# Kernel tuning notes

Hardware: AMD Instinct MI355X
Metric: run time of the kernel (lower is better)

## Reference

```python
import jax, jax.numpy as jnp
import numpy as np

N_VERTICES = 50000
N_RADIAL = 5
N_ANGULAR = 8
FEATURE_DIM = 64
AMT_TEMPLATES = 64
TEMPLATE_RADIUS = 0.03
ROTATION_DELTA = 1


def create_template_matrix(n_radial, n_angular, radius):
    # Polar grid of template vertices in cartesian coordinates: (R, A, 2)
    radii = radius * (np.arange(1, n_radial + 1) / n_radial)
    angles = 2.0 * np.pi * np.arange(n_angular) / n_angular
    x = radii[:, None] * np.cos(angles)[None, :]
    y = radii[:, None] * np.sin(angles)[None, :]
    return np.stack([x, y], axis=-1).astype(np.float32)


def define_interpolation_coefficients(template_matrix):
    # Gaussian interpolation prior (concrete instance of the abstract method),
    # normalized over all template vertices. Shape: (R, A, R, A)
    R, A, _ = template_matrix.shape
    flat = template_matrix.reshape(R * A, 2)
    d2 = ((flat[:, None, :] - flat[None, :, :]) ** 2).sum(-1)  # (RA, RA)
    sigma = TEMPLATE_RADIUS / N_RADIAL
    w = np.exp(-d2 / (2.0 * sigma ** 2))
    w = w / w.sum(axis=1, keepdims=True)
    return w.reshape(R, A, R, A).astype(np.float32)


def setup_inputs() -> dict:
    key = jax.random.key(0)
    k1, k2, k3, k4, k5, k6, k7 = jax.random.split(key, 7)
    mesh_signal = jax.random.normal(k1, (N_VERTICES, FEATURE_DIM), dtype=jnp.float32)
    # barycentric coordinates: [..., 0] = vertex index (stored as float),
    # [..., 1] = barycentric weight summing to 1 over the 3 triangle corners
    idx = jax.random.randint(k2, (N_VERTICES, N_RADIAL, N_ANGULAR, 3), 0, N_VERTICES)
    w = jax.random.uniform(k3, (N_VERTICES, N_RADIAL, N_ANGULAR, 3), dtype=jnp.float32)
    w = w / jnp.sum(w, axis=-1, keepdims=True)
    bary_coordinates = jnp.stack([idx.astype(jnp.float32), w], axis=-1)
    neighbor_weights = jax.random.normal(
        k4, (AMT_TEMPLATES, N_RADIAL, N_ANGULAR, FEATURE_DIM), dtype=jnp.float32) * 0.05
    center_weights = jax.random.normal(
        k5, (AMT_TEMPLATES, 1, FEATURE_DIM), dtype=jnp.float32) * 0.05
    bias = jax.random.normal(k6, (AMT_TEMPLATES,), dtype=jnp.float32) * 0.05
    tmpl = create_template_matrix(N_RADIAL, N_ANGULAR, TEMPLATE_RADIUS)
    interp_coeff = jnp.asarray(
        define_interpolation_coefficients(tmpl).reshape(N_RADIAL, N_ANGULAR, N_RADIAL * N_ANGULAR))
    return {
        "mesh_signal": mesh_signal,
        "bary_coordinates": bary_coordinates,
        "neighbor_weights": neighbor_weights,
        "center_weights": center_weights,
        "bias": bias,
        "interp_coeff": interp_coeff,
    }


def reference(mesh_signal, bary_coordinates, neighbor_weights, center_weights, bias, interp_coeff):
    N, R, A, _, _ = bary_coordinates.shape
    C = mesh_signal.shape[-1]
    T = neighbor_weights.shape[0]

    # ---- patch operator: barycentric gather + interpolation ----
    idx = bary_coordinates[..., 0].astype(jnp.int32)          # (N, R, A, 3)
    bw = bary_coordinates[..., 1]                              # (N, R, A, 3)
    gathered = mesh_signal[idx]                                # (N, R, A, 3, C)
    interp = jnp.sum(bw[..., None] * gathered, axis=-2)        # (N, R, A, C)

    # ---- prior: matvec with interpolation coefficients ----
    # original: (N,1,1,C,RA) matvec (R,A,RA) -> (N,R,A,C)
    ms = interp.reshape(N, R * A, C)                           # (N, RA, C)
    interp = jnp.einsum('nmc,ram->nrac', ms, interp_coeff)     # (N, R, A, C)

    # ---- center fold: einsum('si,tji->sjt') ----
    conv_center = jnp.einsum('nc,tjc->njt', mesh_signal, center_weights)  # (N, 1, T)

    # ---- neighbor fold over rotations ----
    # roll(interp, shift=r, axis=angular) . W == interp . roll(W, shift=-r, axis=angular)
    rotations = np.arange(0, A, ROTATION_DELTA)
    w_rot = jnp.stack([jnp.roll(neighbor_weights, -int(r), axis=2) for r in rotations])  # (O, T, R, A, C)
    conv_neighbor = jnp.einsum('nrac,otrac->not', interp, w_rot) + bias                  # (N, O, T)

    return jax.nn.relu(conv_center + conv_neighbor)
```

## Files before the change

### kernel.cpp

```cpp
#include <hip/hip_runtime.h>
#include <hip/hip_bf16.h>

#define N_V   50000
#define KTOT  2624
#define NOUT  512
#define NKB   41
#define BM    128
#define BN    256
#define KT32  82

typedef short v8s __attribute__((ext_vector_type(8)));
typedef float v4f __attribute__((ext_vector_type(4)));
typedef unsigned int v4u __attribute__((ext_vector_type(4)));
typedef unsigned short u16;
typedef unsigned int u32;

__device__ __forceinline__ u16 f2bf(float f) {
    u32 u = __float_as_uint(f);
    return (u16)((u + 0x7FFFu + ((u >> 16) & 1u)) >> 16);
}

__device__ __forceinline__ void gl2lds(const u16* g, u16* l) {
    __builtin_amdgcn_global_load_lds(
        (const __attribute__((address_space(1))) u32*)(uintptr_t)g,
        (__attribute__((address_space(3))) u32*)(uintptr_t)l, 16, 0, 0);
}

__device__ __forceinline__ u32 ipair(u32 pa, u32 pb, u32 pc, float w0, float w1, float w2) {
    float a0 = __uint_as_float(pa << 16), a1 = __uint_as_float(pa & 0xffff0000u);
    float b0 = __uint_as_float(pb << 16), b1 = __uint_as_float(pb & 0xffff0000u);
    float c0 = __uint_as_float(pc << 16), c1 = __uint_as_float(pc & 0xffff0000u);
    float r0 = w0 * a0 + w1 * b0 + w2 * c0;
    float r1 = w0 * a1 + w1 * b1 + w2 * c1;
    return __builtin_amdgcn_perm(__float_as_uint(r1) + 0x8000u,
                                 __float_as_uint(r0) + 0x8000u, 0x07060302u);
}

__global__ void cast_ms(const float* __restrict__ ms, u16* __restrict__ msb,
                        u16* __restrict__ Xc) {
    int i = (blockIdx.x * 256 + threadIdx.x) * 4;
    float4 v = *reinterpret_cast<const float4*>(ms + i);
    ushort4 o;
    o.x = f2bf(v.x); o.y = f2bf(v.y); o.z = f2bf(v.z); o.w = f2bf(v.w);
    *reinterpret_cast<ushort4*>(msb + i) = o;
    if (Xc) {
        int n = i >> 6, c = i & 63;
        *reinterpret_cast<ushort4*>(Xc + (size_t)n * KTOT + 2560 + c) = o;
    }
}

__global__ void build_w2(const float* __restrict__ nw, const float* __restrict__ cw,
                         const float* __restrict__ coeff, u16* __restrict__ w2) {
    int l = blockIdx.x * 256 + threadIdx.x;
    if (l >= NOUT * KTOT) return;
    int j = l / KTOT, k = l - j * KTOT;
    int o = j >> 6, t = j & 63;
    u16 v;
    if (k >= 2560) {
        v = f2bf(cw[t * 64 + (k - 2560)]);
    } else {
        int m = k >> 6, c = k & 63;
        float s = 0.f;
        #pragma unroll
        for (int ra = 0; ra < 40; ++ra) {
            int r = ra >> 3, a = ra & 7;
            s += coeff[ra * 40 + m] * nw[((t * 5 + r) * 8 + ((a + o) & 7)) * 64 + c];
        }
        v = f2bf(s);
    }
    w2[l] = v;
}

__global__ void build_x(const float* __restrict__ bary, const u16* __restrict__ msb,
                        u16* __restrict__ X) {
    u32 t = blockIdx.x * 256 + threadIdx.x;
    u32 n = t / 160u;
    u32 rem = t - n * 160u;
    u32 m = rem >> 2, j = rem & 3;
    const float* bb = bary + (size_t)n * 240 + m * 6;
    float2 p0 = *(const float2*)(bb);
    float2 p1 = *(const float2*)(bb + 2);
    float2 p2 = *(const float2*)(bb + 4);
    u32 jb = j * 32u;
    u32 o0 = ((u32)(int)p0.x) * 128u + jb;
    u32 o1 = ((u32)(int)p1.x) * 128u + jb;
    u32 o2 = ((u32)(int)p2.x) * 128u + jb;
    const char* mb = (const char*)msb;
    v4u a0 = *(const v4u*)(mb + o0), b0 = *(const v4u*)(mb + o0 + 16);
    v4u a1 = *(const v4u*)(mb + o1), b1 = *(const v4u*)(mb + o1 + 16);
    v4u a2 = *(const v4u*)(mb + o2), b2 = *(const v4u*)(mb + o2 + 16);
    v4u c0, c1;
    #pragma unroll
    for (int e = 0; e < 4; ++e) {
        c0[e] = ipair(a0[e], a1[e], a2[e], p0.y, p1.y, p2.y);
        c1[e] = ipair(b0[e], b1[e], b2[e], p0.y, p1.y, p2.y);
    }
    char* xp = (char*)X + (size_t)n * (KTOT * 2) + m * 128 + jb;
    *(v4u*)xp = c0;
    *(v4u*)(xp + 16) = c1;
}

#define WBAR(N) asm volatile("s_waitcnt vmcnt(" #N ")\n\ts_barrier" ::: "memory")

__global__ __launch_bounds__(512, 2)
void gemm3(const u16* __restrict__ X, const u16* __restrict__ w2,
           const float* __restrict__ bias, float* __restrict__ out) {
    extern __shared__ char lds[];

    const int tid  = threadIdx.x;
    const int lane = tid & 63, wave = tid >> 6;
    const int l15  = lane & 15, q = lane >> 4;
    const int wm   = wave >> 2, wn = wave & 3;

    const int id = blockIdx.x;
    const int p  = (id & 7) + 8 * (id >> 4);
    const int by = (id >> 3) & 1;
    if (p >= 196) return;
    const int row0 = p * 256, col0 = by * 256;

    u32 aoff[2], boff[2];
    #pragma unroll
    for (int h = 0; h < 2; ++h) {
        int slot = (wave * 2 + h) * 64 + lane;
        int row  = slot >> 2, b = slot & 3;
        int g    = b ^ ((row >> 1) & 3);
        int grow = row0 + row; if (grow > N_V - 1) grow = N_V - 1;
        aoff[h] = (u32)grow * (u32)KTOT + (u32)(g * 8);
        boff[h] = (u32)(col0 + row) * (u32)KTOT + (u32)(g * 8);
    }

    const int sw = (l15 >> 1) & 3;
    const u32 a_rd0 = (u32)(wm * 128 + l15) * 64u + (u32)((q ^ sw) * 16);
    const u32 b_rd0 = (u32)(wn * 64  + l15) * 64u + (u32)((q ^ sw) * 16);

    v4f acc[8][4];
    #pragma unroll
    for (int mi = 0; mi < 8; ++mi)
        #pragma unroll
        for (int ni = 0; ni < 4; ++ni)
            acc[mi][ni] = (v4f){0.f, 0.f, 0.f, 0.f};

#define STG(T, BUF) do { \
    const u32 _ko = (u32)(T) * 32u; \
    _Pragma("unroll") \
    for (int _h = 0; _h < 2; ++_h) { \
        gl2lds(X  + aoff[_h] + _ko, (u16*)(lds + (BUF) * 16384 + (wave * 2 + _h) * 1024)); \
        gl2lds(w2 + boff[_h] + _ko, (u16*)(lds + 65536 + (BUF) * 16384 + (wave * 2 + _h) * 1024)); \
    } } while (0)

#define CMP(BUF) do { \
    const char* _ap = lds + (BUF) * 16384; \
    const char* _bp = lds + 65536 + (BUF) * 16384; \
    v8s _bf[4], _af[8]; \
    _Pragma("unroll") \
    for (int _ni = 0; _ni < 4; ++_ni) _bf[_ni] = *(const v8s*)(_bp + b_rd0 + _ni * 1024); \
    _Pragma("unroll") \
    for (int _mi = 0; _mi < 8; ++_mi) _af[_mi] = *(const v8s*)(_ap + a_rd0 + _mi * 1024); \
    __builtin_amdgcn_s_setprio(1); \
    _Pragma("unroll") \
    for (int _mi = 0; _mi < 8; ++_mi) \
        _Pragma("unroll") \
        for (int _ni = 0; _ni < 4; ++_ni) \
            acc[_mi][_ni] = __builtin_amdgcn_mfma_f32_16x16x32_bf16( \
                _af[_mi], _bf[_ni], acc[_mi][_ni], 0, 0, 0); \
    __builtin_amdgcn_s_setprio(0); \
} while (0)

    STG(0, 0); STG(1, 1); STG(2, 2);

    #pragma unroll 1
    for (int t = 0; t < KT32 - 3; ++t) {
        WBAR(8);
        STG(t + 3, (t + 3) & 3);
        CMP(t & 3);
    }
    WBAR(8); CMP(3);
    WBAR(4); CMP(0);
    WBAR(0); CMP(1);

#undef STG
#undef CMP

    float bv[4];
    #pragma unroll
    for (int ni = 0; ni < 4; ++ni) bv[ni] = bias[ni * 16 + l15];
    #pragma unroll
    for (int mi = 0; mi < 8; ++mi) {
        int rbase = row0 + wm * 128 + mi * 16 + q * 4;
        #pragma unroll
        for (int ni = 0; ni < 4; ++ni) {
            int cg = col0 + wn * 64 + ni * 16 + l15;
            #pragma unroll
            for (int rg = 0; rg < 4; ++rg) {
                int rr = rbase + rg;
                if (rr < N_V) {
                    float v = acc[mi][ni][rg] + bv[ni];
                    out[(size_t)rr * NOUT + cg] = v > 0.f ? v : 0.f;
                }
            }
        }
    }
}

__global__ __launch_bounds__(512, 4)
void gemm2(const u16* __restrict__ X, const u16* __restrict__ w2,
           const float* __restrict__ bias, float* __restrict__ out) {
    __shared__ u16 At[BM * 64];
    __shared__ u16 Bt[BN * 64];

    const int tid  = threadIdx.x;
    const int lane = tid & 63, wave = tid >> 6;
    const int l15  = lane & 15, q = lane >> 4;
    const int wm   = wave >> 2, wn = wave & 3;

    const int id = blockIdx.x;
    const int p  = (id & 7) + 8 * (id >> 4);
    const int by = (id >> 3) & 1;
    if (p >= 391) return;
    const int row0 = p * BM, col0 = by * BN;

    u32 aoff[2];
    #pragma unroll
    for (int h = 0; h < 2; ++h) {
        int slot = wave * 128 + h * 64 + lane;
        int arow = slot >> 3, ablk = (slot & 7) ^ (arow & 7);
        int grow = row0 + arow; if (grow > N_V - 1) grow = N_V - 1;
        aoff[h] = (u32)grow * (u32)KTOT + (u32)(ablk * 8);
    }
    u32 boff[4];
    #pragma unroll
    for (int i = 0; i < 4; ++i) {
        int slot = wave * 256 + i * 64 + lane;
        int brow = slot >> 3, bblk = (slot & 7) ^ (brow & 7);
        boff[i] = (u32)(col0 + brow) * (u32)KTOT + (u32)(bblk * 8);
    }

    const int eq = l15 & 7;
    const u32 a_rd0 = (u32)(wm * 64 + l15) * 128 + (u32)((q ^ eq) * 16);
    const u32 b_rd0 = (u32)(wn * 64 + l15) * 128 + (u32)((q ^ eq) * 16);

    v4f acc[4][4];
    #pragma unroll
    for (int mi = 0; mi < 4; ++mi)
        #pragma unroll
        for (int ni = 0; ni < 4; ++ni)
            acc[mi][ni] = (v4f){0.f, 0.f, 0.f, 0.f};

    #pragma unroll 1
    for (int kb = 0; kb < NKB; ++kb) {
        __syncthreads();
        #pragma unroll
        for (int h = 0; h < 2; ++h)
            gl2lds(X + aoff[h] + kb * 64, &At[wave * 1024 + h * 512]);
        #pragma unroll
        for (int i = 0; i < 4; ++i)
            gl2lds(w2 + boff[i] + kb * 64, &Bt[wave * 2048 + i * 512]);
        __syncthreads();

        const char* atp = (const char*)At;
        const char* btp = (const char*)Bt;
        #pragma unroll
        for (int s = 0; s < 2; ++s) {
            u32 ao = a_rd0 ^ (u32)(s * 64), bo = b_rd0 ^ (u32)(s * 64);
            v8s a_f[4], b_f[4];
            #pragma unroll
            for (int mi = 0; mi < 4; ++mi) a_f[mi] = *(const v8s*)(atp + ao + mi * 2048);
            #pragma unroll
            for (int ni = 0; ni < 4; ++ni) b_f[ni] = *(const v8s*)(btp + bo + ni * 2048);
            #pragma unroll
            for (int mi = 0; mi < 4; ++mi)
                #pragma unroll
                for (int ni = 0; ni < 4; ++ni)
                    acc[mi][ni] = __builtin_amdgcn_mfma_f32_16x16x32_bf16(
                        a_f[mi], b_f[ni], acc[mi][ni], 0, 0, 0);
        }
    }

    float bv[4];
    #pragma unroll
    for (int ni = 0; ni < 4; ++ni) bv[ni] = bias[ni * 16 + l15];
    #pragma unroll
    for (int mi = 0; mi < 4; ++mi) {
        int rbase = row0 + wm * 64 + mi * 16 + q * 4;
        #pragma unroll
        for (int ni = 0; ni < 4; ++ni) {
            int cg = col0 + wn * 64 + ni * 16 + l15;
            #pragma unroll
            for (int rg = 0; rg < 4; ++rg) {
                int rr = rbase + rg;
                if (rr < N_V) {
                    float v = acc[mi][ni][rg] + bv[ni];
                    out[(size_t)rr * NOUT + cg] = v > 0.f ? v : 0.f;
                }
            }
        }
    }
}

__global__ __launch_bounds__(512, 2)
void gemm_fused(const float* __restrict__ bary, const u16* __restrict__ msb,
                const u16* __restrict__ w2, const float* __restrict__ bias,
                float* __restrict__ out) {
    __shared__ u16 At[BM * 64];
    __shared__ u16 Bt[2 * BN * 64];

    const int tid  = threadIdx.x;
    const int lane = tid & 63, wave = tid >> 6;
    const int l15  = lane & 15, q = lane >> 4;
    const int wm   = wave >> 2, wn = wave & 3;

    const int id  = blockIdx.x;
    const int bx  = id % 391, by = id / 391;
    const int row0 = bx * BM, col0 = by * BN;

    const int ar  = tid >> 2;
    const u32 acb = (u32)(tid & 3) * 32;
    int an = row0 + ar; if (an > N_V - 1) an = N_V - 1;
    const u32* brow = (const u32*)bary + (size_t)an * 240;
    const u32 an_off = (u32)an * 128 + acb;

    const int e_a = ar & 7;
    const u32 at_w0 = (u32)ar * 128 + (u32)(((2 * (tid & 3)) ^ e_a) * 16);
    const u32 at_w1 = at_w0 ^ 16;

    const int eq = l15 & 7;
    const u32 a_rd0 = (u32)(wm * 64 + l15) * 128 + (u32)((q ^ eq) * 16);
    const u32 b_rd0 = (u32)(wn * 64 + l15) * 128 + (u32)((q ^ eq) * 16);

    const int rl = lane >> 3;
    const int bl = (lane & 7) ^ rl;

    v4f acc[4][4];
    #pragma unroll
    for (int mi = 0; mi < 4; ++mi)
        #pragma unroll
        for (int ni = 0; ni < 4; ++ni)
            acc[mi][ni] = (v4f){0.f, 0.f, 0.f, 0.f};

    v4u G0_0a, G0_0b, G0_1a, G0_1b, G0_2a, G0_2b;
    v4u G1_0a, G1_0b, G1_1a, G1_1b, G1_2a, G1_2b;
    v4u B0lo, B0hi, B1lo, B1hi;
    float w00, w01, w02, w10, w11, w12;
    v4u cv0, cv1;

#define BARY_LOAD(DLO, DHI, kc) do { \
    u32 _d0 = ((u32)((kc) * 6)) & ~3u; \
    DLO = *(const v4u*)(brow + _d0); \
    DHI = *(const v4u*)(brow + _d0 + 4); } while (0)

#define DECODE_ISSUE(PAR, BLO, BHI, Ga0, Gb0, Ga1, Gb1, Ga2, Gb2, W0, W1, W2) do { \
    u32 uf0, uw0, uf1, uw1, uf2, uw2; \
    if (PAR) { uf0 = BLO[2]; uw0 = BLO[3]; uf1 = BHI[0]; uw1 = BHI[1]; uf2 = BHI[2]; uw2 = BHI[3]; } \
    else     { uf0 = BLO[0]; uw0 = BLO[1]; uf1 = BLO[2]; uw1 = BLO[3]; uf2 = BHI[0]; uw2 = BHI[1]; } \
    u32 _o0 = ((u32)(int)__uint_as_float(uf0) << 7) + acb; \
    u32 _o1 = ((u32)(int)__uint_as_float(uf1) << 7) + acb; \
    u32 _o2 = ((u32)(int)__uint_as_float(uf2) << 7) + acb; \
    const char* _mb = (const char*)msb; \
    Ga0 = *(const v4u*)(_mb + _o0); Gb0 = *(const v4u*)(_mb + _o0 + 16); \
    Ga1 = *(const v4u*)(_mb + _o1); Gb1 = *(const v4u*)(_mb + _o1 + 16); \
    Ga2 = *(const v4u*)(_mb + _o2); Gb2 = *(const v4u*)(_mb + _o2 + 16); \
    W0 = __uint_as_float(uw0); W1 = __uint_as_float(uw1); W2 = __uint_as_float(uw2); } while (0)

#define CONVERT(Ga0, Gb0, Ga1, Gb1, Ga2, Gb2, W0, W1, W2) do { \
    _Pragma("unroll") \
    for (int _j = 0; _j < 4; ++_j) { \
        cv0[_j] = ipair(Ga0[_j], Ga1[_j], Ga2[_j], W0, W1, W2); \
        cv1[_j] = ipair(Gb0[_j], Gb1[_j], Gb2[_j], W0, W1, W2); } } while (0)

#define BLDS(KB_LD, BUF) do { \
    _Pragma("unroll") \
    for (int _ii = 0; _ii < 4; ++_ii) { \
        int _we = wave * 4 + _ii; \
        u32 _src = (u32)(col0 + _we * 8 + rl) * KTOT + (u32)(KB_LD) * 64 + (u32)(bl * 8); \
        gl2lds(w2 + _src, &Bt[(BUF) * (BN * 64) + _we * 512]); } } while (0)

#define AT_STORE() do { \
    *(v4u*)((char*)At + at_w0) = cv0; \
    *(v4u*)((char*)At + at_w1) = cv1; } while (0)

#define MFMA_STEP(BUF) do { \
    const char* _atp = (const char*)At; \
    const char* _btp = (const char*)Bt + (BUF) * (BN * 64 * 2); \
    _Pragma("unroll") \
    for (int _s = 0; _s < 2; ++_s) { \
        u32 _ao = a_rd0 ^ (u32)(_s * 64), _bo = b_rd0 ^ (u32)(_s * 64); \
        v8s _af[4], _bf[4]; \
        _Pragma("unroll") \
        for (int _mi = 0; _mi < 4; ++_mi) _af[_mi] = *(const v8s*)(_atp + _ao + _mi * 2048); \
        _Pragma("unroll") \
        for (int _ni = 0; _ni < 4; ++_ni) _bf[_ni] = *(const v8s*)(_btp + _bo + _ni * 2048); \
        _Pragma("unroll") \
        for (int _mi = 0; _mi < 4; ++_mi) \
            _Pragma("unroll") \
            for (int _ni = 0; _ni < 4; ++_ni) \
                acc[_mi][_ni] = __builtin_amdgcn_mfma_f32_16x16x32_bf16( \
                    _af[_mi], _bf[_ni], acc[_mi][_ni], 0, 0, 0); } } while (0)

#define BAR2_12() asm volatile("s_waitcnt vmcnt(12) lgkmcnt(0)\ns_barrier" ::: "memory")
#define BAR2_10() asm volatile("s_waitcnt vmcnt(10) lgkmcnt(0)\ns_barrier" ::: "memory")
#define BAR2_6()  asm volatile("s_waitcnt vmcnt(6) lgkmcnt(0)\ns_barrier"  ::: "memory")
#define BAR2_4()  asm volatile("s_waitcnt vmcnt(4) lgkmcnt(0)\ns_barrier"  ::: "memory")
#define BAR2_0()  asm volatile("s_waitcnt vmcnt(0) lgkmcnt(0)\ns_barrier"  ::: "memory")
#define BAR1()    asm volatile("s_barrier" ::: "memory")

    BARY_LOAD(B0lo, B0hi, 0);
    DECODE_ISSUE(0, B0lo, B0hi, G0_0a, G0_0b, G0_1a, G0_1b, G0_2a, G0_2b, w00, w01, w02);
    BARY_LOAD(B1lo, B1hi, 1);
    DECODE_ISSUE(1, B1lo, B1hi, G1_0a, G1_0b, G1_1a, G1_1b, G1_2a, G1_2b, w10, w11, w12);
    BARY_LOAD(B0lo, B0hi, 2);
    BLDS(0, 0);

    #pragma unroll 1
    for (int i = 0; i < 20; ++i) {
        {
            const int kb = 2 * i;
            CONVERT(G0_0a, G0_0b, G0_1a, G0_1b, G0_2a, G0_2b, w00, w01, w02);
            if (kb <= 36) BARY_LOAD(B1lo, B1hi, kb + 3);
            if (kb <= 37) {
                DECODE_ISSUE(0, B0lo, B0hi, G0_0a, G0_0b, G0_1a, G0_1b, G0_2a, G0_2b,
                             w00, w01, w02);
            } else if (kb == 38) {
                G0_0a = *(const v4u*)((const char*)msb + an_off);
                G0_0b = *(const v4u*)((const char*)msb + an_off + 16);
            }
            BAR1();
            BLDS(kb + 1, 1);
            AT_STORE();
            if (kb <= 36) BAR2_12(); else BAR2_6();
            MFMA_STEP(0);
        }
        {
            const int kb = 2 * i + 1;
            CONVERT(G1_0a, G1_0b, G1_1a, G1_1b, G1_2a, G1_2b, w10, w11, w12);
            if (kb <= 36) BARY_LOAD(B0lo, B0hi, kb + 3);
            if (kb <= 37)
                DECODE_ISSUE(1, B1lo, B1hi, G1_0a, G1_0b, G1_1a, G1_1b, G1_2a, G1_2b,
                             w10, w11, w12);
            BAR1();
            BLDS(kb + 1, 0);
            AT_STORE();
            if (kb <= 36) BAR2_12();
            else if (kb == 37) BAR2_10();
            else BAR2_4();
            MFMA_STEP(1);
        }
    }
    {
        cv0 = G0_0a; cv1 = G0_0b;
        BAR1();
        AT_STORE();
        BAR2_0();
        MFMA_STEP(0);
    }

    float bv[4];
    #pragma unroll
    for (int ni = 0; ni < 4; ++ni) bv[ni] = bias[ni * 16 + l15];
    #pragma unroll
    for (int mi = 0; mi < 4; ++mi) {
        int rbase = row0 + wm * 64 + mi * 16 + q * 4;
        #pragma unroll
        for (int ni = 0; ni < 4; ++ni) {
            int cg = col0 + wn * 64 + ni * 16 + l15;
            #pragma unroll
            for (int rg = 0; rg < 4; ++rg) {
                int rr = rbase + rg;
                if (rr < N_V) {
                    float v = acc[mi][ni][rg] + bv[ni];
                    out[(size_t)rr * NOUT + cg] = v > 0.f ? v : 0.f;
                }
            }
        }
    }
}

extern "C" void kernel_launch(void* const* d_in, const int* in_sizes, int n_in,
                              void* d_out, int out_size, void* d_ws, size_t ws_size,
                              hipStream_t stream) {
    const float* ms    = (const float*)d_in[0];
    const float* bary  = (const float*)d_in[1];
    const float* nw    = (const float*)d_in[2];
    const float* cw    = (const float*)d_in[3];
    const float* bias  = (const float*)d_in[4];
    const float* coeff = (const float*)d_in[5];
    float* out = (float*)d_out;

    u16* msb = (u16*)d_ws;
    u16* w2  = (u16*)((char*)d_ws + 6400000);
    const size_t x_off  = 9087104;
    const size_t x_need = x_off + (size_t)N_V * KTOT * 2;
    u16* X = (u16*)((char*)d_ws + x_off);

    if (ws_size >= x_need) {
        static int dyn_ok = -1;
        if (dyn_ok < 0) {
            dyn_ok = (hipFuncSetAttribute((const void*)gemm3,
                          hipFuncAttributeMaxDynamicSharedMemorySize,
                          131072) == hipSuccess) ? 1 : 0;
        }
        cast_ms<<<3125, 256, 0, stream>>>(ms, msb, X);
        build_w2<<<(NOUT * KTOT + 255) / 256, 256, 0, stream>>>(nw, cw, coeff, w2);
        build_x<<<31250, 256, 0, stream>>>(bary, msb, X);
        if (dyn_ok)
            gemm3<<<400, 512, 131072, stream>>>(X, w2, bias, out);
        else
            gemm2<<<784, 512, 0, stream>>>(X, w2, bias, out);
    } else {
        cast_ms<<<3125, 256, 0, stream>>>(ms, msb, (u16*)nullptr);
        build_w2<<<(NOUT * KTOT + 255) / 256, 256, 0, stream>>>(nw, cw, coeff, w2);
        gemm_fused<<<782, 512, 0, stream>>>(bary, msb, w2, bias, out);
    }
}
```

Measured before the change: 464.9 us.

## Split GEMM K-step into two phases with 3-stage LDS ring

```diff
diff --git a/kernel.cpp b/kernel.cpp
--- a/kernel.cpp
+++ b/kernel.cpp
@@ -7,7 +7,7 @@
 #define NKB   41
 #define BM    128
 #define BN    256
-#define KT32  82
+#define NT32  82
 
 typedef short v8s __attribute__((ext_vector_type(8)));
 typedef float v4f __attribute__((ext_vector_type(4)));
@@ -100,10 +100,13 @@
     *(v4u*)(xp + 16) = c1;
 }
 
-#define WBAR(N) asm volatile("s_waitcnt vmcnt(" #N ")\n\ts_barrier" ::: "memory")
+#define WB6() asm volatile("s_waitcnt vmcnt(6)\n\ts_barrier" ::: "memory")
+#define WB4() asm volatile("s_waitcnt vmcnt(4)\n\ts_barrier" ::: "memory")
+#define WB0() asm volatile("s_waitcnt vmcnt(0)\n\ts_barrier" ::: "memory")
+#define BARO() asm volatile("s_barrier" ::: "memory")
 
 __global__ __launch_bounds__(512, 2)
-void gemm3(const u16* __restrict__ X, const u16* __restrict__ w2,
+void gemm5(const u16* __restrict__ X, const u16* __restrict__ w2,
            const float* __restrict__ bias, float* __restrict__ out) {
     extern __shared__ char lds[];
 
@@ -120,13 +123,13 @@
 
     u32 aoff[2], boff[2];
     #pragma unroll
-    for (int h = 0; h < 2; ++h) {
-        int slot = (wave * 2 + h) * 64 + lane;
-        int row  = slot >> 2, b = slot & 3;
-        int g    = b ^ ((row >> 1) & 3);
+    for (int i = 0; i < 2; ++i) {
+        int s   = i * 512 + tid;
+        int row = s >> 2, b = s & 3;
+        int g   = b ^ ((row >> 1) & 3);
         int grow = row0 + row; if (grow > N_V - 1) grow = N_V - 1;
-        aoff[h] = (u32)grow * (u32)KTOT + (u32)(g * 8);
-        boff[h] = (u32)(col0 + row) * (u32)KTOT + (u32)(g * 8);
+        aoff[i] = (u32)grow * (u32)KTOT + (u32)(g * 8);
+        boff[i] = (u32)(col0 + row) * (u32)KTOT + (u32)(g * 8);
     }
 
     const int sw = (l15 >> 1) & 3;
@@ -140,46 +143,69 @@
         for (int ni = 0; ni < 4; ++ni)
             acc[mi][ni] = (v4f){0.f, 0.f, 0.f, 0.f};
 
-#define STG(T, BUF) do { \
-    const u32 _ko = (u32)(T) * 32u; \
-    _Pragma("unroll") \
-    for (int _h = 0; _h < 2; ++_h) { \
-        gl2lds(X  + aoff[_h] + _ko, (u16*)(lds + (BUF) * 16384 + (wave * 2 + _h) * 1024)); \
-        gl2lds(w2 + boff[_h] + _ko, (u16*)(lds + 65536 + (BUF) * 16384 + (wave * 2 + _h) * 1024)); \
-    } } while (0)
-
-#define CMP(BUF) do { \
-    const char* _ap = lds + (BUF) * 16384; \
-    const char* _bp = lds + 65536 + (BUF) * 16384; \
-    v8s _bf[4], _af[8]; \
-    _Pragma("unroll") \
-    for (int _ni = 0; _ni < 4; ++_ni) _bf[_ni] = *(const v8s*)(_bp + b_rd0 + _ni * 1024); \
-    _Pragma("unroll") \
-    for (int _mi = 0; _mi < 8; ++_mi) _af[_mi] = *(const v8s*)(_ap + a_rd0 + _mi * 1024); \
+#define STG_P(T, BUF, PH) do { \
+    gl2lds(X  + aoff[PH] + (u32)(T) * 32u, \
+           (u16*)(lds + (BUF) * 32768 + (PH) * 8192 + wave * 1024)); \
+    gl2lds(w2 + boff[PH] + (u32)(T) * 32u, \
+           (u16*)(lds + (BUF) * 32768 + 16384 + (PH) * 8192 + wave * 1024)); \
+} while (0)
+
+#define PH0(BUF) do { \
+    const char* _ap = lds + (BUF) * 32768; \
+    const char* _bp = _ap + 16384; \
+    _Pragma("unroll") \
+    for (int _ni = 0; _ni < 4; ++_ni) bf[_ni] = *(const v8s*)(_bp + b_rd0 + _ni * 1024); \
+    _Pragma("unroll") \
+    for (int _mi = 0; _mi < 4; ++_mi) af[_mi] = *(const v8s*)(_ap + a_rd0 + _mi * 1024); \
     __builtin_amdgcn_s_setprio(1); \
     _Pragma("unroll") \
-    for (int _mi = 0; _mi < 8; ++_mi) \
+    for (int _mi = 0; _mi < 4; ++_mi) \
         _Pragma("unroll") \
         for (int _ni = 0; _ni < 4; ++_ni) \
             acc[_mi][_ni] = __builtin_amdgcn_mfma_f32_16x16x32_bf16( \
-                _af[_mi], _bf[_ni], acc[_mi][_ni], 0, 0, 0); \
+                af[_mi], bf[_ni], acc[_mi][_ni], 0, 0, 0); \
     __builtin_amdgcn_s_setprio(0); \
 } while (0)
 
-    STG(0, 0); STG(1, 1); STG(2, 2);
-
+#define PH1(BUF) do { \
+    const char* _ap = lds + (BUF) * 32768; \
+    _Pragma("unroll") \
+    for (int _mi = 0; _mi < 4; ++_mi) af[_mi] = *(const v8s*)(_ap + a_rd0 + (4 + _mi) * 1024); \
+    __builtin_amdgcn_s_setprio(1); \
+    _Pragma("unroll") \
+    for (int _mi = 0; _mi < 4; ++_mi) \
+        _Pragma("unroll") \
+        for (int _ni = 0; _ni < 4; ++_ni) \
+            acc[4 + _mi][_ni] = __builtin_amdgcn_mfma_f32_16x16x32_bf16( \
+                af[_mi], bf[_ni], acc[4 + _mi][_ni], 0, 0, 0); \
+    __builtin_amdgcn_s_setprio(0); \
+} while (0)
+
+    v8s af[4], bf[4];
+
+    STG_P(0, 0, 0); STG_P(0, 0, 1);
+    STG_P(1, 1, 0); STG_P(1, 1, 1);
+
+    int bt = 0;
     #pragma unroll 1
-    for (int t = 0; t < KT32 - 3; ++t) {
-        WBAR(8);
-        STG(t + 3, (t + 3) & 3);
-        CMP(t & 3);
-    }
-    WBAR(8); CMP(3);
-    WBAR(4); CMP(0);
-    WBAR(0); CMP(1);
-
-#undef STG
-#undef CMP
+    for (int t = 0; t < NT32 - 2; ++t) {
+        const int b2 = bt ? bt - 1 : 2;
+        STG_P(t + 2, b2, 0);
+        WB6();
+        PH0(bt);
+        BARO();
+        STG_P(t + 2, b2, 1);
+        PH1(bt);
+        BARO();
+        bt = (bt == 2) ? 0 : bt + 1;
+    }
+    WB4(); PH0(bt); BARO(); PH1(bt); BARO();
+    bt = (bt == 2) ? 0 : bt + 1;
+    WB0(); PH0(bt); BARO(); PH1(bt);
+
+#undef STG_P
+#undef PH0
+#undef PH1
 
     float bv[4];
     #pragma unroll
@@ -494,15 +520,15 @@
     if (ws_size >= x_need) {
         static int dyn_ok = -1;
         if (dyn_ok < 0) {
-            dyn_ok = (hipFuncSetAttribute((const void*)gemm3,
+            dyn_ok = (hipFuncSetAttribute((const void*)gemm5,
                           hipFuncAttributeMaxDynamicSharedMemorySize,
-                          131072) == hipSuccess) ? 1 : 0;
+                          98304) == hipSuccess) ? 1 : 0;
         }
         cast_ms<<<3125, 256, 0, stream>>>(ms, msb, X);
         build_w2<<<(NOUT * KTOT + 255) / 256, 256, 0, stream>>>(nw, cw, coeff, w2);
         build_x<<<31250, 256, 0, stream>>>(bary, msb, X);
         if (dyn_ok)
-            gemm3<<<400, 512, 131072, stream>>>(X, w2, bias, out);
+            gemm5<<<400, 512, 98304, stream>>>(X, w2, bias, out);
         else
             gemm2<<<784, 512, 0, stream>>>(X, w2, bias, out);
     } else {
```

Result: faster. 455.0 us (-2.1%).
